# Performance work log

Hardware: AMD Instinct MI355X
Metric: run time of the kernel (lower is better)

## Reference

```python
import jax, jax.numpy as jnp
import numpy as np

B, S, IN_DIM = 8, 4096, 1024
N_SLOTS, SLOT_DIM, N_HEADS, CHUNK, TOP_K = 64, 256, 4, 16, 3
EPS_LN = 1e-5


def setup_inputs() -> dict:
    key = jax.random.key(0)
    ks = jax.random.split(key, 8)
    std = 0.02
    return {
        "x": jax.random.normal(ks[0], (B, S, IN_DIM), jnp.float32),
        "slot_memory": jax.random.normal(ks[1], (1, N_SLOTS, SLOT_DIM), jnp.float32) * std,
        "slot_keys": jax.random.normal(ks[2], (N_SLOTS, SLOT_DIM), jnp.float32) * std,
        "W_in": jax.random.normal(ks[3], (IN_DIM, SLOT_DIM), jnp.float32) / np.sqrt(IN_DIM).astype(np.float32),
        "W_write": jax.random.normal(ks[4], (SLOT_DIM, SLOT_DIM), jnp.float32) / np.sqrt(SLOT_DIM).astype(np.float32),
        "W_gate": jax.random.normal(ks[5], (2 * SLOT_DIM, 1), jnp.float32) / np.sqrt(2 * SLOT_DIM).astype(np.float32),
        "b_gate": jnp.zeros((1,), jnp.float32),
        "W_out": jax.random.normal(ks[6], (SLOT_DIM, IN_DIM), jnp.float32) / np.sqrt(SLOT_DIM).astype(np.float32),
        "ln_in_scale": jnp.ones((IN_DIM,), jnp.float32),
        "ln_in_bias": jnp.zeros((IN_DIM,), jnp.float32),
        "ln_s_scale": jnp.ones((SLOT_DIM,), jnp.float32),
        "ln_s_bias": jnp.zeros((SLOT_DIM,), jnp.float32),
    }


def _layer_norm(x, scale, bias):
    m = jnp.mean(x, axis=-1, keepdims=True)
    v = jnp.mean((x - m) ** 2, axis=-1, keepdims=True)
    return (x - m) * jax.lax.rsqrt(v + EPS_LN) * scale + bias


def _l2norm(x):
    n = jnp.sqrt(jnp.sum(x * x, axis=-1, keepdims=True))
    return x / jnp.maximum(n, 1e-12)  # matches F.normalize eps


def _forward(x, slot_memory, slot_keys, W_in, W_write, W_gate, b_gate, W_out,
             ln_in_scale, ln_in_bias, ln_s_scale, ln_s_bias):
    Bx, Sx, _ = x.shape
    hd = SLOT_DIM // N_HEADS
    slots0 = jnp.broadcast_to(slot_memory, (Bx, N_SLOTS, SLOT_DIM))

    # ---- batched read attention over slots ----
    q = _layer_norm(x, ln_in_scale, ln_in_bias) @ W_in          # (B,S,D)
    qh = q.reshape(Bx, Sx, N_HEADS, hd)
    kh = slots0.reshape(Bx, N_SLOTS, N_HEADS, hd)               # k == v == slots
    scores = jnp.einsum('bshd,bnhd->bhsn', qh, kh) * (hd ** -0.5)
    attn = jax.nn.softmax(scores, axis=-1)                      # (B,H,S,N)
    read = jnp.einsum('bhsn,bnhd->bshd', attn, kh).reshape(Bx, Sx, SLOT_DIM)

    # ---- sequential chunked top-k gather/scatter slot write ----
    key_norms = _l2norm(slot_keys)                              # (N,D)
    b_idx = jnp.arange(Bx)[:, None]

    def chunk_step(slots, chunk):                               # chunk: (B,C,D)
        summary = chunk.mean(axis=1)                            # (B,D)
        match = _l2norm(summary) @ key_norms.T                  # (B,N) cosine sim
        _, top_idx = jax.lax.top_k(match, TOP_K)                # (B,K)
        wv = summary @ W_write                                  # (B,D)
        sel = jnp.take_along_axis(slots, top_idx[:, :, None], axis=1)  # (B,K,D)
        gate = jax.nn.sigmoid(
            jnp.concatenate([sel.mean(axis=1), wv], axis=-1) @ W_gate + b_gate)  # (B,1)
        g = gate[:, None, :]
        new_vals = (1.0 - g) * sel + g * wv[:, None, :]         # (B,K,D)
        return slots.at[b_idx, top_idx].set(new_vals), None

    chunks = read.reshape(Bx, Sx // CHUNK, CHUNK, SLOT_DIM).transpose(1, 0, 2, 3)
    slots_f, _ = jax.lax.scan(chunk_step, slots0, chunks)
    new_slots = _layer_norm(slots_f, ln_s_scale, ln_s_bias)

    out = read @ W_out                                          # dropout is identity in eval
    return out, new_slots


def reference(x, slot_memory, slot_keys, W_in, W_write, W_gate, b_gate, W_out,
              ln_in_scale, ln_in_bias, ln_s_scale, ln_s_bias):
    return _forward(x, slot_memory, slot_keys, W_in, W_write, W_gate, b_gate, W_out,
                    ln_in_scale, ln_in_bias, ln_s_scale, ln_s_bias)
```

## Files before the change

### kernel.cpp

```cpp
#include <hip/hip_runtime.h>

typedef __attribute__((ext_vector_type(8))) short s8v;
typedef __attribute__((ext_vector_type(4))) float f4v;

#define PADG 72

union U8 { unsigned u[4]; s8v s; };

__device__ __forceinline__ void gload16(const void* g, void* l) {
  __builtin_amdgcn_global_load_lds((const __attribute__((address_space(1))) void*)g,
                                   (__attribute__((address_space(3))) void*)l, 16, 0, 0);
}

__device__ __forceinline__ unsigned short f2bf(float f) {
  unsigned u = __float_as_uint(f);
  u += 0x7fffu + ((u >> 16) & 1u);
  return (unsigned short)(u >> 16);
}
__device__ __forceinline__ unsigned short f2bfc(float f) {
  return (unsigned short)((__float_as_uint(f) + 0x8000u) >> 16);
}
__device__ __forceinline__ float bf2f(unsigned short h) {
  return __uint_as_float(((unsigned)h) << 16);
}
__device__ __forceinline__ void split2(float x0, float x1, unsigned& hp, unsigned& lp) {
  unsigned t0 = __float_as_uint(x0) + 0x8000u;
  unsigned t1 = __float_as_uint(x1) + 0x8000u;
  float h0 = __uint_as_float(t0 & 0xFFFF0000u);
  float h1 = __uint_as_float(t1 & 0xFFFF0000u);
  float l0 = x0 - h0, l1 = x1 - h1;
  hp = __builtin_amdgcn_perm(t1, t0, 0x07060302u);
  lp = __builtin_amdgcn_perm(__float_as_uint(l1) + 0x8000u,
                             __float_as_uint(l0) + 0x8000u, 0x07060302u);
}
__device__ __forceinline__ unsigned pack2(float a, float b) {
  return __builtin_amdgcn_perm(__float_as_uint(b) + 0x8000u,
                               __float_as_uint(a) + 0x8000u, 0x07060302u);
}
__device__ __forceinline__ f4v vmax4(f4v a, f4v b) {
  f4v r; r[0]=fmaxf(a[0],b[0]); r[1]=fmaxf(a[1],b[1]); r[2]=fmaxf(a[2],b[2]); r[3]=fmaxf(a[3],b[3]); return r;
}
__device__ __forceinline__ f4v shflxor4(f4v v, int m) {
  f4v r; r[0]=__shfl_xor(v[0],m); r[1]=__shfl_xor(v[1],m); r[2]=__shfl_xor(v[2],m); r[3]=__shfl_xor(v[3],m); return r;
}
__device__ __forceinline__ f4v exp4(f4v v) {
  f4v r; r[0]=__expf(v[0]); r[1]=__expf(v[1]); r[2]=__expf(v[2]); r[3]=__expf(v[3]); return r;
}

__global__ void k_prep(const float* __restrict__ W_in, const float* __restrict__ lnis,
                       const float* __restrict__ lnib, const float* __restrict__ W_out,
                       const float* __restrict__ skeys, const float* __restrict__ smem0,
                       const float* __restrict__ wgate,
                       unsigned short* __restrict__ wth, unsigned short* __restrict__ wtl,
                       unsigned short* __restrict__ wot, float* __restrict__ keyn,
                       float* __restrict__ d0, float* __restrict__ uvec, float* __restrict__ vvec)
{
  __shared__ float pr[4];
  const int bid = blockIdx.x, tid = threadIdx.x;
  if (bid < 1024) {
    int idx = bid * 256 + tid;
    int n = idx >> 10, k = idx & 1023;
    float val = lnis[k] * W_in[k * 256 + n];
    unsigned short h = f2bf(val);
    wth[idx] = h;
    wtl[idx] = f2bf(val - bf2f(h));
  } else if (bid < 2048) {
    int idx = (bid - 1024) * 256 + tid;
    int n = idx >> 8, k = idx & 255;
    wot[idx] = f2bf(W_out[k * 1024 + n]);
  } else if (bid == 2048) {
    float su = 0.f, sv = 0.f;
    for (int i = 0; i < 1024; ++i) {
      float wv_ = W_in[i * 256 + tid];
      su += lnis[i] * wv_;
      sv += lnib[i] * wv_;
    }
    uvec[tid] = su; vvec[tid] = sv;
  } else {
    int n = bid - 2049;
    float sk = skeys[n * 256 + tid];
    float sq = sk * sk;
    #pragma unroll
    for (int m = 32; m; m >>= 1) sq += __shfl_xor(sq, m);
    if ((tid & 63) == 0) pr[tid >> 6] = sq;
    __syncthreads();
    float tot = pr[0] + pr[1] + pr[2] + pr[3];
    keyn[n * 256 + tid] = sk * (1.0f / fmaxf(sqrtf(tot), 1e-12f));
    float pd = smem0[n * 256 + tid] * wgate[tid];
    #pragma unroll
    for (int m = 32; m; m >>= 1) pd += __shfl_xor(pd, m);
    __syncthreads();
    if ((tid & 63) == 0) pr[tid >> 6] = pd;
    __syncthreads();
    if (tid == 0) d0[n] = pr[0] + pr[1] + pr[2] + pr[3];
  }
}

__global__ __launch_bounds__(512, 4) void k_gemm1(const float* __restrict__ x,
    const unsigned short* __restrict__ wth, const unsigned short* __restrict__ wtl,
    const float* __restrict__ uvec, const float* __restrict__ vvec,
    float* __restrict__ q)
{
  __shared__ unsigned short Ah[128 * PADG], Al[128 * PADG];
  __shared__ unsigned short Bh[128 * PADG], Bl[128 * PADG];
  __shared__ float uls[128], vls[128];
  __shared__ float mls[128], rls[128];
  const int tid = threadIdx.x;
  const int w = tid >> 6, lane = tid & 63;
  const int wm = w >> 2, wn = w & 3;
  const int bid = blockIdx.x;
  const int mblk = (bid >> 4) * 8 + (bid & 7), nblk = (bid >> 3) & 1;
  const int row0 = mblk * 128, n0 = nblk * 128;
  if (tid < 128) { uls[tid] = uvec[n0 + tid]; vls[tid] = vvec[n0 + tid]; }
  f4v zz = {0.f, 0.f, 0.f, 0.f};
  f4v acc[4][2];
  #pragma unroll
  for (int i = 0; i < 4; ++i)
    #pragma unroll
    for (int j = 0; j < 2; ++j) acc[i][j] = zz;
  const int rowA = tid >> 2, kqA = (tid & 3) * 16;
  float ps = 0.f, pss = 0.f;
  for (int kt = 0; kt < 16; ++kt) {
    const int k0 = kt * 64;
    {
      const float* src = x + (size_t)(row0 + rowA) * 1024 + k0 + kqA;
      float vv[16];
      #pragma unroll
      for (int i = 0; i < 4; ++i) *(f4v*)(vv + 4 * i) = *(const f4v*)(src + 4 * i);
      unsigned hp[8], lp[8];
      #pragma unroll
      for (int i = 0; i < 8; ++i) {
        ps += vv[2 * i] + vv[2 * i + 1];
        pss += vv[2 * i] * vv[2 * i] + vv[2 * i + 1] * vv[2 * i + 1];
        split2(vv[2 * i], vv[2 * i + 1], hp[i], lp[i]);
      }
      uint4* dh = (uint4*)&Ah[rowA * PADG + kqA];
      uint4* dl = (uint4*)&Al[rowA * PADG + kqA];
      dh[0] = make_uint4(hp[0], hp[1], hp[2], hp[3]);
      dh[1] = make_uint4(hp[4], hp[5], hp[6], hp[7]);
      dl[0] = make_uint4(lp[0], lp[1], lp[2], lp[3]);
      dl[1] = make_uint4(lp[4], lp[5], lp[6], lp[7]);
      const unsigned short* sh = wth + (size_t)(n0 + rowA) * 1024 + k0 + kqA;
      const unsigned short* sl = wtl + (size_t)(n0 + rowA) * 1024 + k0 + kqA;
      *(s8v*)&Bh[rowA * PADG + kqA] = *(const s8v*)sh;
      *(s8v*)&Bh[rowA * PADG + kqA + 8] = *(const s8v*)(sh + 8);
      *(s8v*)&Bl[rowA * PADG + kqA] = *(const s8v*)sl;
      *(s8v*)&Bl[rowA * PADG + kqA + 8] = *(const s8v*)(sl + 8);
    }
    __syncthreads();
    #pragma unroll
    for (int kk = 0; kk < 64; kk += 32) {
      const int kb = kk + (lane >> 4) * 8;
      s8v ah[4], al[4], bh[2], bl[2];
      #pragma unroll
      for (int mi = 0; mi < 4; ++mi) {
        const int rr = (wm * 64 + mi * 16 + (lane & 15)) * PADG + kb;
        ah[mi] = *(const s8v*)&Ah[rr];
        al[mi] = *(const s8v*)&Al[rr];
      }
      #pragma unroll
      for (int ni = 0; ni < 2; ++ni) {
        const int ccv = (wn * 32 + ni * 16 + (lane & 15)) * PADG + kb;
        bh[ni] = *(const s8v*)&Bh[ccv];
        bl[ni] = *(const s8v*)&Bl[ccv];
      }
      #pragma unroll
      for (int mi = 0; mi < 4; ++mi)
        #pragma unroll
        for (int ni = 0; ni < 2; ++ni) {
          acc[mi][ni] = __builtin_amdgcn_mfma_f32_16x16x32_bf16(ah[mi], bh[ni], acc[mi][ni], 0, 0, 0);
          acc[mi][ni] = __builtin_amdgcn_mfma_f32_16x16x32_bf16(ah[mi], bl[ni], acc[mi][ni], 0, 0, 0);
          acc[mi][ni] = __builtin_amdgcn_mfma_f32_16x16x32_bf16(al[mi], bh[ni], acc[mi][ni], 0, 0, 0);
        }
    }
    __syncthreads();
  }
  {
    float s0 = ps, s1 = pss;
    s0 += __shfl_xor(s0, 1); s1 += __shfl_xor(s1, 1);
    s0 += __shfl_xor(s0, 2); s1 += __shfl_xor(s1, 2);
    if ((tid & 3) == 0) {
      float mean = s0 * (1.0f / 1024.0f);
      mls[rowA] = mean;
      rls[rowA] = rsqrtf(s1 * (1.0f / 1024.0f) - mean * mean + 1e-5f);
    }
  }
  __syncthreads();
  #pragma unroll
  for (int mi = 0; mi < 4; ++mi)
    #pragma unroll
    for (int j = 0; j < 4; ++j) {
      const int lr = wm * 64 + mi * 16 + (lane >> 4) * 4 + j;
      const int r = row0 + lr;
      const float mv = mls[lr], rv = rls[lr];
      #pragma unroll
      for (int ni = 0; ni < 2; ++ni) {
        const int lc = wn * 32 + ni * 16 + (lane & 15);
        q[(size_t)r * 256 + n0 + lc] = rv * acc[mi][ni][j] - rv * mv * uls[lc] + vls[lc];
      }
    }
}

__global__ __launch_bounds__(512, 2) void k_attn(const float* __restrict__ q,
    const float* __restrict__ smem0, unsigned short* __restrict__ readb,
    float* __restrict__ summ)
{
  __shared__ float Kf[64 * 256];
  __shared__ float Pl[8][16 * 68];
  __shared__ float csm[8][64];
  const int tid = threadIdx.x;
  const int w = tid >> 6, lane = tid & 63;
  const int h = w & 3;
  const int l15 = lane & 15, kq = lane >> 4;

  {
    const int base = tid * 32;
    #pragma unroll
    for (int i = 0; i < 8; ++i)
      *(f4v*)&Kf[base + i * 4] = *(const f4v*)&smem0[base + i * 4];
  }
  __syncthreads();

  s8v bsh[4][2], bsl[4][2], bpv[4][2];
  #pragma unroll
  for (int nt = 0; nt < 4; ++nt)
    #pragma unroll
    for (int ks = 0; ks < 2; ++ks) {
      const float* src = &Kf[(nt * 16 + l15) * 256 + h * 64 + ks * 32 + kq * 8];
      float tmp[8];
      *(f4v*)tmp = *(const f4v*)src; *(f4v*)(tmp + 4) = *(const f4v*)(src + 4);
      U8 uh, ul;
      #pragma unroll
      for (int j = 0; j < 4; ++j) split2(tmp[2 * j], tmp[2 * j + 1], uh.u[j], ul.u[j]);
      bsh[nt][ks] = uh.s;
      bsl[nt][ks] = ul.s;
      U8 up;
      #pragma unroll
      for (int j = 0; j < 4; ++j)
        up.u[j] = pack2(Kf[(ks * 32 + kq * 8 + 2 * j) * 256 + h * 64 + nt * 16 + l15],
                        Kf[(ks * 32 + kq * 8 + 2 * j + 1) * 256 + h * 64 + nt * 16 + l15]);
      bpv[nt][ks] = up.s;
    }

  const int g0 = blockIdx.x * 8 + (w >> 2) * 4;
  f4v qv[2][4];
  {
    #pragma unroll
    for (int ks = 0; ks < 2; ++ks) {
      const float* qp = q + (size_t)(g0 * 16 + l15) * 256 + h * 64 + ks * 32 + kq * 8;
      qv[0][ks * 2] = *(const f4v*)qp;
      qv[0][ks * 2 + 1] = *(const f4v*)(qp + 4);
    }
  }
  #pragma unroll
  for (int i = 0; i < 4; ++i) {
    const int cur = i & 1, nxt = cur ^ 1;
    if (i < 3) {
      const int gn = g0 + i + 1;
      #pragma unroll
      for (int ks = 0; ks < 2; ++ks) {
        const float* qp = q + (size_t)(gn * 16 + l15) * 256 + h * 64 + ks * 32 + kq * 8;
        qv[nxt][ks * 2] = *(const f4v*)qp;
        qv[nxt][ks * 2 + 1] = *(const f4v*)(qp + 4);
      }
    }
    const int g = g0 + i;
    s8v ah[2], al[2];
    #pragma unroll
    for (int ks = 0; ks < 2; ++ks) {
      float tmp[8];
      *(f4v*)tmp = qv[cur][ks * 2]; *(f4v*)(tmp + 4) = qv[cur][ks * 2 + 1];
      U8 uh, ul;
      #pragma unroll
      for (int j = 0; j < 4; ++j) split2(tmp[2 * j], tmp[2 * j + 1], uh.u[j], ul.u[j]);
      ah[ks] = uh.s; al[ks] = ul.s;
    }
    f4v zz = {0.f, 0.f, 0.f, 0.f};
    f4v sacc[4] = {zz, zz, zz, zz};
    #pragma unroll
    for (int ks = 0; ks < 2; ++ks)
      #pragma unroll
      for (int nt = 0; nt < 4; ++nt) {
        sacc[nt] = __builtin_amdgcn_mfma_f32_16x16x32_bf16(ah[ks], bsh[nt][ks], sacc[nt], 0, 0, 0);
        sacc[nt] = __builtin_amdgcn_mfma_f32_16x16x32_bf16(ah[ks], bsl[nt][ks], sacc[nt], 0, 0, 0);
        sacc[nt] = __builtin_amdgcn_mfma_f32_16x16x32_bf16(al[ks], bsh[nt][ks], sacc[nt], 0, 0, 0);
      }
    #pragma unroll
    for (int nt = 0; nt < 4; ++nt) sacc[nt] = sacc[nt] * 0.125f;
    f4v mx = vmax4(vmax4(sacc[0], sacc[1]), vmax4(sacc[2], sacc[3]));
    #pragma unroll
    for (int m = 1; m <= 8; m <<= 1) mx = vmax4(mx, shflxor4(mx, m));
    f4v p[4];
    f4v psum = zz;
    #pragma unroll
    for (int nt = 0; nt < 4; ++nt) { p[nt] = exp4(sacc[nt] - mx); psum = psum + p[nt]; }
    #pragma unroll
    for (int m = 1; m <= 8; m <<= 1) psum = psum + shflxor4(psum, m);
    f4v rs;
    rs[0] = 1.0f / psum[0]; rs[1] = 1.0f / psum[1];
    rs[2] = 1.0f / psum[2]; rs[3] = 1.0f / psum[3];
    #pragma unroll
    for (int nt = 0; nt < 4; ++nt) p[nt] = p[nt] * rs;
    float cs4[4];
    #pragma unroll
    for (int nt = 0; nt < 4; ++nt) {
      cs4[nt] = p[nt][0] + p[nt][1] + p[nt][2] + p[nt][3];
      cs4[nt] += __shfl_xor(cs4[nt], 16);
      cs4[nt] += __shfl_xor(cs4[nt], 32);
    }
    if (kq == 0) {
      #pragma unroll
      for (int nt = 0; nt < 4; ++nt) csm[w][nt * 16 + l15] = cs4[nt];
    }
    #pragma unroll
    for (int nt = 0; nt < 4; ++nt)
      #pragma unroll
      for (int j = 0; j < 4; ++j)
        Pl[w][(kq * 4 + j) * 68 + nt * 16 + l15] = p[nt][j];
    s8v pa[2];
    #pragma unroll
    for (int ks = 0; ks < 2; ++ks) {
      const float* pp = &Pl[w][l15 * 68 + ks * 32 + kq * 8];
      float tmp[8];
      *(f4v*)tmp = *(const f4v*)pp; *(f4v*)(tmp + 4) = *(const f4v*)(pp + 4);
      U8 up;
      #pragma unroll
      for (int j = 0; j < 4; ++j) up.u[j] = pack2(tmp[2 * j], tmp[2 * j + 1]);
      pa[ks] = up.s;
    }
    f4v racc[4] = {zz, zz, zz, zz};
    #pragma unroll
    for (int ks = 0; ks < 2; ++ks)
      #pragma unroll
      for (int nt = 0; nt < 4; ++nt)
        racc[nt] = __builtin_amdgcn_mfma_f32_16x16x32_bf16(pa[ks], bpv[nt][ks], racc[nt], 0, 0, 0);
    const int rowbase = (g >> 8) * 4096 + (g & 255) * 16;
    #pragma unroll
    for (int nt = 0; nt < 4; ++nt)
      #pragma unroll
      for (int j = 0; j < 4; ++j)
        readb[(size_t)(rowbase + kq * 4 + j) * 256 + h * 64 + nt * 16 + l15] = f2bfc(racc[nt][j]);
    float s = 0.f;
    #pragma unroll 8
    for (int n = 0; n < 64; ++n) s += csm[w][n] * Kf[n * 256 + h * 64 + lane];
    summ[(size_t)g * 256 + h * 64 + lane] = s * (1.0f / 16.0f);
  }
}

__global__ void k_match(const float* __restrict__ summ, const float* __restrict__ keyn,
                        const float* __restrict__ Wwr, const float* __restrict__ wgate,
                        int* __restrict__ top3, float* __restrict__ wv,
                        float* __restrict__ wg2, float* __restrict__ dwv)
{
  __shared__ float sm[8][256];
  __shared__ float nrm_inv[8];
  __shared__ float mtch[8][64];
  __shared__ float redA[8][4], redB[8][4];
  const int tid = threadIdx.x, lane = tid & 63, w = tid >> 6;
  const int gbase = blockIdx.x * 8;
  #pragma unroll
  for (int gi = 0; gi < 8; ++gi) sm[gi][tid] = summ[(size_t)(gbase + gi) * 256 + tid];
  __syncthreads();
  {
    #pragma unroll
    for (int pass = 0; pass < 2; ++pass) {
      const int gi = w + pass * 4;
      float ss = 0.f;
      #pragma unroll
      for (int i = 0; i < 4; ++i) { float vv_ = sm[gi][lane + i * 64]; ss += vv_ * vv_; }
      #pragma unroll
      for (int m = 32; m; m >>= 1) ss += __shfl_xor(ss, m);
      if (lane == 0) nrm_inv[gi] = 1.0f / fmaxf(sqrtf(ss), 1e-12f);
    }
  }
  __syncthreads();
  {
    const int n = tid >> 2, qq = tid & 3;
    float mac[8] = {0.f, 0.f, 0.f, 0.f, 0.f, 0.f, 0.f, 0.f};
    const float* kp = keyn + n * 256 + qq * 64;
    for (int d = 0; d < 64; ++d) {
      float kv = kp[d];
      int dd = qq * 64 + d;
      #pragma unroll
      for (int gi = 0; gi < 8; ++gi) mac[gi] += sm[gi][dd] * kv;
    }
    #pragma unroll
    for (int gi = 0; gi < 8; ++gi) {
      float v2_ = mac[gi];
      v2_ += __shfl_xor(v2_, 1);
      v2_ += __shfl_xor(v2_, 2);
      if (qq == 0) mtch[gi][n] = v2_ * nrm_inv[gi];
    }
  }
  __syncthreads();
  {
    #pragma unroll
    for (int pass = 0; pass < 2; ++pass) {
      const int gi = w + pass * 4;
      float vorig = mtch[gi][lane];
      #pragma unroll
      for (int it = 0; it < 3; ++it) {
        float rv = vorig; int ri = lane;
        #pragma unroll
        for (int m = 32; m; m >>= 1) {
          float ov = __shfl_xor(rv, m); int oi = __shfl_xor(ri, m);
          if (ov > rv || (ov == rv && oi < ri)) { rv = ov; ri = oi; }
        }
        if (lane == 0) top3[(gbase + gi) * 4 + it] = ri;
        if (lane == ri) vorig = -3.0e38f;
      }
    }
  }
  float wva[8] = {0.f, 0.f, 0.f, 0.f, 0.f, 0.f, 0.f, 0.f};
  for (int d = 0; d < 256; ++d) {
    float ww = Wwr[(size_t)d * 256 + tid];
    #pragma unroll
    for (int gi = 0; gi < 8; ++gi) wva[gi] += sm[gi][d] * ww;
  }
  const float g1 = wgate[tid], g2 = wgate[256 + tid];
  #pragma unroll
  for (int gi = 0; gi < 8; ++gi) {
    wv[(size_t)(gbase + gi) * 256 + tid] = wva[gi];
    float p2 = wva[gi] * g2, p1 = wva[gi] * g1;
    #pragma unroll
    for (int m = 32; m; m >>= 1) { p2 += __shfl_xor(p2, m); p1 += __shfl_xor(p1, m); }
    if (lane == 0) { redA[gi][w] = p2; redB[gi][w] = p1; }
  }
  __syncthreads();
  if (tid < 8) {
    wg2[gbase + tid] = redA[tid][0] + redA[tid][1] + redA[tid][2] + redA[tid][3];
    dwv[gbase + tid] = redB[tid][0] + redB[tid][1] + redB[tid][2] + redB[tid][3];
  }
}

__global__ __launch_bounds__(1024) void k_scan(const float* __restrict__ d0,
    const int* __restrict__ top3, const float* __restrict__ wg2, const float* __restrict__ dwv,
    const float* __restrict__ bgate, const float* __restrict__ wv,
    const float* __restrict__ smem0, const float* __restrict__ lnss,
    const float* __restrict__ lnsb, float* __restrict__ outns)
{
  __shared__ float Wl[256][64];
  __shared__ float pn[64];
  __shared__ float wvs[32][256];
  __shared__ float gls[256];
  __shared__ int   pprm[256][4];
  __shared__ float dsl[64];
  const int bb = blockIdx.x, tid = threadIdx.x;
  const int lane = tid & 63;

  int ixA[4], iyA[4], izA[4];
  if (tid < 64) {
    const float bg = bgate[0];
    const float L2E = 1.4426950408889634f;
    #pragma unroll
    for (int j = 0; j < 4; ++j) {
      const int c = j * 64 + tid;
      int4 t3 = *(const int4*)&top3[(bb * 256 + c) * 4];
      ixA[j] = t3.x; iyA[j] = t3.y; izA[j] = t3.z;
      pprm[c][0] = t3.x | (t3.y << 6) | (t3.z << 12);
      pprm[c][1] = __float_as_int(-(wg2[bb * 256 + c] + bg) * L2E);
      pprm[c][2] = __float_as_int(dwv[bb * 256 + c]);
      pprm[c][3] = 0;
    }
    dsl[tid] = d0[tid];
  }
  __syncthreads();

  if (tid == 0) {
    const float COEFN = -0.48089834696298783f;
    #pragma unroll 2
    for (int c = 0; c < 256; ++c) {
      const int4 pr = *(const int4*)&pprm[c][0];
      const int i0 = pr.x & 63, i1 = (pr.x >> 6) & 63, i2 = (pr.x >> 12) & 63;
      const float wz = __int_as_float(pr.y);
      const float dv = __int_as_float(pr.z);
      const float a = dsl[i0], b = dsl[i1], d2 = dsl[i2];
      const float s3 = a + b + d2;
      const float e = __builtin_amdgcn_exp2f(fmaf(s3, COEFN, wz));
      const float g = __builtin_amdgcn_rcpf(1.0f + e);
      gls[c] = g;
      dsl[i0] = fmaf(g, dv - a, a);
      dsl[i1] = fmaf(g, dv - b, b);
      dsl[i2] = fmaf(g, dv - d2, d2);
    }
  }
  __syncthreads();

  if (tid < 64) {
    float running = 1.0f;
    #pragma unroll
    for (int j = 3; j >= 0; --j) {
      #pragma unroll 1
      for (int sl = 63; sl >= 0; --sl) {
        const int a0 = __builtin_amdgcn_readlane(ixA[j], sl);
        const int a1 = __builtin_amdgcn_readlane(iyA[j], sl);
        const int a2 = __builtin_amdgcn_readlane(izA[j], sl);
        const float gv = gls[j * 64 + sl];
        const bool hit = (lane == a0) | (lane == a1) | (lane == a2);
        Wl[j * 64 + sl][lane] = hit ? gv * running : 0.f;
        running = hit ? running * (1.0f - gv) : running;
      }
    }
    pn[lane] = running;
  }
  __syncthreads();

  const int n = tid >> 4, dq = tid & 15;
  float acc[16];
  {
    const float p = pn[n];
    const float* v0p = smem0 + n * 256 + dq * 16;
    #pragma unroll
    for (int i = 0; i < 16; i += 4) {
      f4v v0 = *(const f4v*)(v0p + i);
      acc[i] = p * v0[0]; acc[i + 1] = p * v0[1];
      acc[i + 2] = p * v0[2]; acc[i + 3] = p * v0[3];
    }
  }
  const int rr = tid >> 5, cc8 = (tid & 31) * 8;
  for (int ct = 0; ct < 8; ++ct) {
    __syncthreads();
    {
      const float* src = wv + (size_t)(bb * 256 + ct * 32 + rr) * 256 + cc8;
      *(f4v*)&wvs[rr][cc8] = *(const f4v*)src;
      *(f4v*)&wvs[rr][cc8 + 4] = *(const f4v*)(src + 4);
    }
    __syncthreads();
    #pragma unroll 1
    for (int cc = 0; cc < 32; ++cc) {
      const float coef = Wl[ct * 32 + cc][n];
      if (coef != 0.f) {
        const float* wp = &wvs[cc][dq * 16];
        #pragma unroll
        for (int i4 = 0; i4 < 4; ++i4) {
          f4v wq = *(const f4v*)(wp + i4 * 4);
          acc[i4 * 4 + 0] += coef * wq[0];
          acc[i4 * 4 + 1] += coef * wq[1];
          acc[i4 * 4 + 2] += coef * wq[2];
          acc[i4 * 4 + 3] += coef * wq[3];
        }
      }
    }
  }

  float s1 = 0.f;
  #pragma unroll
  for (int i = 0; i < 16; ++i) s1 += acc[i];
  #pragma unroll
  for (int m = 1; m < 16; m <<= 1) s1 += __shfl_xor(s1, m);
  const float mean = s1 * (1.0f / 256.0f);
  float s2 = 0.f;
  #pragma unroll
  for (int i = 0; i < 16; ++i) { float dd = acc[i] - mean; s2 += dd * dd; }
  #pragma unroll
  for (int m = 1; m < 16; m <<= 1) s2 += __shfl_xor(s2, m);
  const float rstd = rsqrtf(s2 * (1.0f / 256.0f) + 1e-5f);
  {
    const int base = (bb * 64 + n) * 256 + dq * 16;
    #pragma unroll
    for (int i = 0; i < 16; ++i) {
      int dd = dq * 16 + i;
      outns[base + i] = (acc[i] - mean) * rstd * lnss[dd] + lnsb[dd];
    }
  }
}

__global__ __launch_bounds__(512, 2) void k_gemm2(const unsigned short* __restrict__ a,
    const unsigned short* __restrict__ wot, float* __restrict__ out)
{
  __shared__ unsigned short As[128 * 64];
  __shared__ unsigned short Bs[256 * 64];
  const int tid = threadIdx.x;
  const int w = tid >> 6, lane = tid & 63;
  const int wm = w >> 2, wn = w & 3;
  const int mblk = blockIdx.x >> 2, nblk = blockIdx.x & 3;
  const int row0 = mblk * 128, n0 = nblk * 256;
  f4v zz = {0.f, 0.f, 0.f, 0.f};
  f4v acc[4][4];
  #pragma unroll
  for (int i = 0; i < 4; ++i)
    #pragma unroll
    for (int j = 0; j < 4; ++j) acc[i][j] = zz;
  const int grow = w * 8 + (lane >> 3);
  const int gswz = ((lane & 7) ^ (lane >> 3)) << 3;
  for (int kt = 0; kt < 4; ++kt) {
    const int k0 = kt * 64;
    gload16(a + (size_t)(row0 + grow) * 256 + k0 + gswz,        &As[w * 512]);
    gload16(a + (size_t)(row0 + 64 + grow) * 256 + k0 + gswz,   &As[4096 + w * 512]);
    #pragma unroll
    for (int i = 0; i < 4; ++i)
      gload16(wot + (size_t)(n0 + i * 64 + grow) * 256 + k0 + gswz, &Bs[i * 4096 + w * 512]);
    __syncthreads();
    #pragma unroll
    for (int kk = 0; kk < 64; kk += 32) {
      const int kb = kk + (lane >> 4) * 8;
      s8v af[4], bf[4];
      #pragma unroll
      for (int mi = 0; mi < 4; ++mi) {
        const int r = wm * 64 + mi * 16 + (lane & 15);
        af[mi] = *(const s8v*)&As[r * 64 + (kb ^ ((r & 7) * 8))];
      }
      #pragma unroll
      for (int ni = 0; ni < 4; ++ni) {
        const int r = wn * 64 + ni * 16 + (lane & 15);
        bf[ni] = *(const s8v*)&Bs[r * 64 + (kb ^ ((r & 7) * 8))];
      }
      #pragma unroll
      for (int mi = 0; mi < 4; ++mi)
        #pragma unroll
        for (int ni = 0; ni < 4; ++ni)
          acc[mi][ni] = __builtin_amdgcn_mfma_f32_16x16x32_bf16(af[mi], bf[ni], acc[mi][ni], 0, 0, 0);
    }
    __syncthreads();
  }
  #pragma unroll
  for (int mi = 0; mi < 4; ++mi)
    #pragma unroll
    for (int j = 0; j < 4; ++j) {
      const int r = row0 + wm * 64 + mi * 16 + (lane >> 4) * 4 + j;
      #pragma unroll
      for (int ni = 0; ni < 4; ++ni) {
        const int cidx = wn * 64 + ni * 16 + (lane & 15);
        out[(size_t)r * 1024 + n0 + cidx] = acc[mi][ni][j];
      }
    }
}

extern "C" void kernel_launch(void* const* d_in, const int* in_sizes, int n_in,
                              void* d_out, int out_size, void* d_ws, size_t ws_size,
                              hipStream_t stream) {
  const float* x      = (const float*)d_in[0];
  const float* smem   = (const float*)d_in[1];
  const float* skeys  = (const float*)d_in[2];
  const float* W_in   = (const float*)d_in[3];
  const float* W_wr   = (const float*)d_in[4];
  const float* wgate  = (const float*)d_in[5];
  const float* bgate  = (const float*)d_in[6];
  const float* W_out  = (const float*)d_in[7];
  const float* lnis   = (const float*)d_in[8];
  const float* lnib   = (const float*)d_in[9];
  const float* lnss   = (const float*)d_in[10];
  const float* lnsb   = (const float*)d_in[11];
  (void)in_sizes; (void)n_in; (void)out_size; (void)ws_size;

  char* ws = (char*)d_ws;
  float*          q_buf = (float*)(ws + 0);
  unsigned short* readb = (unsigned short*)(ws + 134217728);
  float*          summ  = (float*)(ws + 150994944);
  float*          wv    = (float*)(ws + 153092096);
  unsigned short* wth   = (unsigned short*)(ws + 155189248);
  unsigned short* wtl   = (unsigned short*)(ws + 155713536);
  unsigned short* wot   = (unsigned short*)(ws + 156237824);
  float*          keyn  = (float*)(ws + 156762112);
  float*          uvec  = (float*)(ws + 157089792);
  float*          vvec  = (float*)(ws + 157090816);
  float*          d0    = (float*)(ws + 157091840);
  int*            top3  = (int*)(ws + 157092096);
  float*          wg2   = (float*)(ws + 157124864);
  float*          dwv   = (float*)(ws + 157133056);

  float* out   = (float*)d_out;
  float* outns = out + 33554432;

  k_prep<<<dim3(2113), dim3(256), 0, stream>>>(W_in, lnis, lnib, W_out, skeys, smem, wgate,
                                               wth, wtl, wot, keyn, d0, uvec, vvec);
  k_gemm1<<<dim3(512), dim3(512), 0, stream>>>(x, wth, wtl, uvec, vvec, q_buf);
  k_attn<<<dim3(256), dim3(512), 0, stream>>>(q_buf, smem, readb, summ);
  k_match<<<dim3(256), dim3(256), 0, stream>>>(summ, keyn, W_wr, wgate, top3, wv, wg2, dwv);
  k_scan<<<dim3(8), dim3(1024), 0, stream>>>(d0, top3, wg2, dwv, bgate, wv, smem, lnss, lnsb, outns);
  k_gemm2<<<dim3(1024), dim3(512), 0, stream>>>(readb, wot, out);
}
```

Measured before the change: 301.8 us.

## Drop LDS slot staging in attention kernel and double grid with fewer chunks per warp

Removes the 64KB shared-memory copy of the slot matrix from the attention kernel, reading slot values straight from global memory (cache-resident) instead, which frees LDS so more blocks can be resident (launch bounds raised to 4 blocks/CU). Each warp group now handles 2 chunks instead of 4, with the grid doubled to 512 blocks and the software prefetch of the next q tile replaced by loading both tiles up front. The trade-off is more redundant global reads of the slot matrix per block (including strided per-element reads for the transposed operand and the summary loop) and tighter register limits from the higher occupancy target.

```diff
diff --git a/kernel.cpp b/kernel.cpp
--- a/kernel.cpp
+++ b/kernel.cpp
@@ -201,32 +201,23 @@
     }
 }
 
-__global__ __launch_bounds__(512, 2) void k_attn(const float* __restrict__ q,
+__global__ __launch_bounds__(512, 4) void k_attn(const float* __restrict__ q,
     const float* __restrict__ smem0, unsigned short* __restrict__ readb,
     float* __restrict__ summ)
 {
-  __shared__ float Kf[64 * 256];
   __shared__ float Pl[8][16 * 68];
   __shared__ float csm[8][64];
   const int tid = threadIdx.x;
   const int w = tid >> 6, lane = tid & 63;
-  const int h = w & 3;
+  const int cl = w >> 2, h = w & 3;
   const int l15 = lane & 15, kq = lane >> 4;
 
-  {
-    const int base = tid * 32;
-    #pragma unroll
-    for (int i = 0; i < 8; ++i)
-      *(f4v*)&Kf[base + i * 4] = *(const f4v*)&smem0[base + i * 4];
-  }
-  __syncthreads();
-
   s8v bsh[4][2], bsl[4][2], bpv[4][2];
   #pragma unroll
   for (int nt = 0; nt < 4; ++nt)
     #pragma unroll
     for (int ks = 0; ks < 2; ++ks) {
-      const float* src = &Kf[(nt * 16 + l15) * 256 + h * 64 + ks * 32 + kq * 8];
+      const float* src = smem0 + (nt * 16 + l15) * 256 + h * 64 + ks * 32 + kq * 8;
       float tmp[8];
       *(f4v*)tmp = *(const f4v*)src; *(f4v*)(tmp + 4) = *(const f4v*)(src + 4);
       U8 uh, ul;
@@ -237,39 +228,30 @@
       U8 up;
       #pragma unroll
       for (int j = 0; j < 4; ++j)
-        up.u[j] = pack2(Kf[(ks * 32 + kq * 8 + 2 * j) * 256 + h * 64 + nt * 16 + l15],
-                        Kf[(ks * 32 + kq * 8 + 2 * j + 1) * 256 + h * 64 + nt * 16 + l15]);
+        up.u[j] = pack2(smem0[(ks * 32 + kq * 8 + 2 * j) * 256 + h * 64 + nt * 16 + l15],
+                        smem0[(ks * 32 + kq * 8 + 2 * j + 1) * 256 + h * 64 + nt * 16 + l15]);
       bpv[nt][ks] = up.s;
     }
 
-  const int g0 = blockIdx.x * 8 + (w >> 2) * 4;
+  const int g0 = blockIdx.x * 4 + cl * 2;
   f4v qv[2][4];
-  {
+  #pragma unroll
+  for (int i = 0; i < 2; ++i) {
     #pragma unroll
     for (int ks = 0; ks < 2; ++ks) {
-      const float* qp = q + (size_t)(g0 * 16 + l15) * 256 + h * 64 + ks * 32 + kq * 8;
-      qv[0][ks * 2] = *(const f4v*)qp;
-      qv[0][ks * 2 + 1] = *(const f4v*)(qp + 4);
-    }
-  }
-  #pragma unroll
-  for (int i = 0; i < 4; ++i) {
-    const int cur = i & 1, nxt = cur ^ 1;
-    if (i < 3) {
-      const int gn = g0 + i + 1;
-      #pragma unroll
-      for (int ks = 0; ks < 2; ++ks) {
-        const float* qp = q + (size_t)(gn * 16 + l15) * 256 + h * 64 + ks * 32 + kq * 8;
-        qv[nxt][ks * 2] = *(const f4v*)qp;
-        qv[nxt][ks * 2 + 1] = *(const f4v*)(qp + 4);
-      }
-    }
+      const float* qp = q + (size_t)((g0 + i) * 16 + l15) * 256 + h * 64 + ks * 32 + kq * 8;
+      qv[i][ks * 2] = *(const f4v*)qp;
+      qv[i][ks * 2 + 1] = *(const f4v*)(qp + 4);
+    }
+  }
+  #pragma unroll
+  for (int i = 0; i < 2; ++i) {
     const int g = g0 + i;
     s8v ah[2], al[2];
     #pragma unroll
     for (int ks = 0; ks < 2; ++ks) {
       float tmp[8];
-      *(f4v*)tmp = qv[cur][ks * 2]; *(f4v*)(tmp + 4) = qv[cur][ks * 2 + 1];
+      *(f4v*)tmp = qv[i][ks * 2]; *(f4v*)(tmp + 4) = qv[i][ks * 2 + 1];
       U8 uh, ul;
       #pragma unroll
       for (int j = 0; j < 4; ++j) split2(tmp[2 * j], tmp[2 * j + 1], uh.u[j], ul.u[j]);
@@ -342,7 +324,7 @@
         readb[(size_t)(rowbase + kq * 4 + j) * 256 + h * 64 + nt * 16 + l15] = f2bfc(racc[nt][j]);
     float s = 0.f;
     #pragma unroll 8
-    for (int n = 0; n < 64; ++n) s += csm[w][n] * Kf[n * 256 + h * 64 + lane];
+    for (int n = 0; n < 64; ++n) s += csm[w][n] * smem0[n * 256 + h * 64 + lane];
     summ[(size_t)g * 256 + h * 64 + lane] = s * (1.0f / 16.0f);
   }
 }
@@ -665,7 +647,7 @@
   k_prep<<<dim3(2113), dim3(256), 0, stream>>>(W_in, lnis, lnib, W_out, skeys, smem, wgate,
                                                wth, wtl, wot, keyn, d0, uvec, vvec);
   k_gemm1<<<dim3(512), dim3(512), 0, stream>>>(x, wth, wtl, uvec, vvec, q_buf);
-  k_attn<<<dim3(256), dim3(512), 0, stream>>>(q_buf, smem, readb, summ);
+  k_attn<<<dim3(512), dim3(512), 0, stream>>>(q_buf, smem, readb, summ);
   k_match<<<dim3(256), dim3(256), 0, stream>>>(summ, keyn, W_wr, wgate, top3, wv, wg2, dwv);
   k_scan<<<dim3(8), dim3(1024), 0, stream>>>(d0, top3, wg2, dwv, bgate, wv, smem, lnss, lnsb, outns);
   k_gemm2<<<dim3(1024), dim3(512), 0, stream>>>(readb, wot, out);
```

Result: slower. 348.9 us (+15.6%).
